# Kernel optimization log

Measured on AMD Instinct MI355X. Metric: run time of the kernel, lower is better.

The kernel has to match this reference:

```python
import jax, jax.numpy as jnp
import numpy as np

N_NODES = 100000


def gcn_conv(x, edge_index, W, b):
    # PyG GCNConv: add self-loops, symmetric normalization, then scatter-add.
    n = x.shape[0]
    loops = jnp.arange(n, dtype=edge_index.dtype)
    src = jnp.concatenate([edge_index[0], loops])
    dst = jnp.concatenate([edge_index[1], loops])
    h = x @ W  # [N, F_out] -- transform before propagate (small GEMM)
    ones = jnp.ones(src.shape[0], dtype=x.dtype)
    deg = jax.ops.segment_sum(ones, dst, num_segments=n)  # in-degree incl. self-loop
    dinv = jnp.where(deg > 0, jax.lax.rsqrt(deg), 0.0)
    norm = dinv[src] * dinv[dst]  # [E+N]
    msg = h[src] * norm[:, None]  # gather + scale, [E+N, F_out]
    out = jax.ops.segment_sum(msg, dst, num_segments=n)  # scatter-add
    return out + b


def setup_inputs() -> dict:
    key = jax.random.key(0)
    k1, k2, k3, k4 = jax.random.split(key, 4)
    d = 128
    x = jax.random.normal(k1, (N_NODES, d), dtype=jnp.float32)
    edge_index = jax.random.randint(k2, (2, 1600000), 0, N_NODES, dtype=jnp.int64)
    scale = 1.0 / np.sqrt(d)
    W1 = jax.random.normal(k3, (d, d), dtype=jnp.float32) * scale
    b1 = jnp.zeros((d,), dtype=jnp.float32)
    W2 = jax.random.normal(k4, (d, d), dtype=jnp.float32) * scale
    b2 = jnp.zeros((d,), dtype=jnp.float32)
    return {"x": x, "edge_index": edge_index, "W1": W1, "b1": b1, "W2": W2, "b2": b2}


def reference(x, edge_index, W1, b1, W2, b2):
    # Layer 1: GCNConv -> relu -> dropout(eval: identity)
    h = jax.nn.relu(gcn_conv(x, edge_index, W1, b1))
    # Layer 2
    h = jax.nn.relu(gcn_conv(h, edge_index, W2, b2))
    return h
```

## Files before the change

### kernel.cpp

```cpp
#include <hip/hip_runtime.h>


#define NFEAT 128
#define BSH 7
#define MAXNB 1024
#define BCAP 4096

typedef __attribute__((ext_vector_type(8))) short s8v;
typedef __attribute__((ext_vector_type(4))) float f4v;

__device__ inline ushort f2bf(float f) {
    union { float f; uint u; } x; x.f = f;
    uint u = x.u;
    return (ushort)((u + 0x7fffu + ((u >> 16) & 1u)) >> 16);
}
__device__ inline float bf16lo(uint u) { union { uint u; float f; } x; x.u = u << 16; return x.f; }
__device__ inline float bf16hi(uint u) { union { uint u; float f; } x; x.u = u & 0xffff0000u; return x.f; }

__device__ inline void upadd(uint4 v, float* a) {
    a[0] += bf16lo(v.x); a[1] += bf16hi(v.x);
    a[2] += bf16lo(v.y); a[3] += bf16hi(v.y);
    a[4] += bf16lo(v.z); a[5] += bf16hi(v.z);
    a[6] += bf16lo(v.w); a[7] += bf16hi(v.w);
}

__global__ __launch_bounds__(256) void k_prep(const float* __restrict__ W1,
                                              const float* __restrict__ W2,
                                              ushort* __restrict__ WT1,
                                              ushort* __restrict__ WT2,
                                              int* __restrict__ gcnt,
                                              ushort* __restrict__ hs, int N) {
    int t = threadIdx.x;
    if (blockIdx.x == 2) {
        for (int i = t; i < MAXNB; i += 256) gcnt[i] = 0;
        if (t < 64) ((uint*)(hs + (size_t)N * NFEAT))[t] = 0;
        return;
    }
    __shared__ float Ls[128][133];
    const float* W = blockIdx.x ? W2 : W1;
    ushort* WT = blockIdx.x ? WT2 : WT1;
#pragma unroll
    for (int i = 0; i < 64; i++) {
        int idx = t + i * 256;
        Ls[idx >> 7][idx & 127] = W[idx];
    }
    __syncthreads();
#pragma unroll
    for (int i = 0; i < 8; i++) {
        int idx = t + i * 256;
        int n = idx >> 4;
        int k8 = (idx & 15) << 3;
        ushort o[8];
#pragma unroll
        for (int j = 0; j < 8; j++) o[j] = f2bf(Ls[k8 + j][n]);
        uint4 pk;
        __builtin_memcpy(&pk, o, 16);
        *(uint4*)&WT[n * 128 + k8] = pk;
    }
}

__global__ __launch_bounds__(256) void k_bscatter(const int* __restrict__ src,
                                                  const int* __restrict__ dst,
                                                  int* __restrict__ gcnt,
                                                  uint* __restrict__ ebuf,
                                                  int E, int NB, int CH) {
    __shared__ int h[MAXNB];
    int t = threadIdx.x;
    for (int i = t; i < NB; i += 256) h[i] = 0;
    __syncthreads();
    int e0 = blockIdx.x * CH;
    int e1 = min(e0 + CH, E);
    for (int e = e0 + t; e < e1; e += 256) atomicAdd(&h[dst[e] >> BSH], 1);
    __syncthreads();
    for (int i = t; i < NB; i += 256) {
        int c = h[i];
        h[i] = c ? (i * BCAP + atomicAdd(&gcnt[i], c)) : 0;
    }
    __syncthreads();
    for (int e = e0 + t; e < e1; e += 256) {
        int d = dst[e];
        int b = d >> BSH;
        int p = atomicAdd(&h[b], 1);
        if (p < (b + 1) * BCAP)
            ebuf[p] = ((uint)src[e] << BSH) | (uint)(d & ((1 << BSH) - 1));
    }
}

__global__ __launch_bounds__(256) void k_fill2(const uint* __restrict__ ebuf,
                                               const int* __restrict__ gcnt,
                                               int* __restrict__ row_ptr,
                                               float* __restrict__ dinv,
                                               int* __restrict__ col,
                                               int N, int E, int NB) {
    __shared__ int cnt[128];
    __shared__ int pre[128];
    __shared__ int sred[256];
    __shared__ int colL[BCAP];
    int b = blockIdx.x;
    int t = threadIdx.x;
    int part = 0;
    for (int j = t; j < b; j += 256) part += gcnt[j];
    sred[t] = part;
    __syncthreads();
    for (int off = 128; off >= 1; off >>= 1) {
        if (t < off) sred[t] += sred[t + off];
        __syncthreads();
    }
    int gb = sred[0];
    int m = min(gcnt[b], BCAP);
    if (t < 128) cnt[t] = 0;
    __syncthreads();
    const uint* eb = ebuf + (size_t)b * BCAP;
    for (int i = t; i < m; i += 256) atomicAdd(&cnt[eb[i] & 127], 1);
    __syncthreads();
    if (t < 128) pre[t] = cnt[t];
    __syncthreads();
    for (int off = 1; off < 128; off <<= 1) {
        int add = (t >= off && t < 128) ? pre[t - off] : 0;
        __syncthreads();
        if (t < 128) pre[t] += add;
        __syncthreads();
    }
    if (t < 128) {
        pre[t] -= cnt[t];
        int node = (b << BSH) + t;
        if (node < N) {
            row_ptr[node] = gb + pre[t];
            dinv[node] = rsqrtf((float)(cnt[t] + 1));
        }
    }
    __syncthreads();
    for (int i = t; i < m; i += 256) {
        uint p = eb[i];
        int pos = atomicAdd(&pre[p & 127], 1);
        colL[pos] = (int)(p >> BSH);
    }
    __syncthreads();
    for (int i = t; i < m; i += 256) col[gb + i] = colL[i];
    if (b == NB - 1 && t == 0) row_ptr[N] = E;
}

__device__ inline ushort* lds_chunk(ushort* base, int r, int c) {
    return base + r * 128 + ((c ^ (r & 15)) << 3);
}

template <bool ABF16>
__global__ __launch_bounds__(256) void k_gemm_mfma(const void* __restrict__ Ap,
                                                   const ushort* __restrict__ WT,
                                                   const float* __restrict__ dinv,
                                                   ushort* __restrict__ hs, int M) {
    __shared__ ushort As[128 * 128];
    __shared__ ushort Bs[128 * 128];
    int t = threadIdx.x;
    int m0 = blockIdx.x * 128;

    {
        const uint4* wt4 = (const uint4*)WT;
#pragma unroll
        for (int i = 0; i < 8; i++) {
            int idx = t + i * 256;
            int n = idx >> 4;
            int c = idx & 15;
            uint4 v = wt4[idx];
            *(uint4*)lds_chunk(Bs, n, c) = v;
        }
    }
    if (ABF16) {
        const ushort* A = (const ushort*)Ap;
#pragma unroll
        for (int i = 0; i < 8; i++) {
            int idx = t + i * 256;
            int r = idx >> 4;
            int c = idx & 15;
            int row = m0 + r;
            uint4 v = make_uint4(0, 0, 0, 0);
            if (row < M) v = *(const uint4*)(A + (size_t)row * NFEAT + (c << 3));
            *(uint4*)lds_chunk(As, r, c) = v;
        }
    } else {
        const float* A = (const float*)Ap;
#pragma unroll
        for (int i = 0; i < 16; i++) {
            int idx = t + i * 256;
            int r = idx >> 5;
            int t5 = idx & 31;
            int c = t5 >> 1;
            int h = t5 & 1;
            int row = m0 + r;
            float4 v = make_float4(0.f, 0.f, 0.f, 0.f);
            if (row < M) v = *(const float4*)(A + (size_t)row * NFEAT + t5 * 4);
            ushort o[4] = {f2bf(v.x), f2bf(v.y), f2bf(v.z), f2bf(v.w)};
            uint2 pk;
            __builtin_memcpy(&pk, o, 8);
            *(uint2*)(lds_chunk(As, r, c) + h * 4) = pk;
        }
    }
    __syncthreads();

    int w = t >> 6, l = t & 63;
    int q = l >> 4, ln = l & 15;
    f4v acc[2][8];
#pragma unroll
    for (int mt = 0; mt < 2; mt++)
#pragma unroll
        for (int nt = 0; nt < 8; nt++) acc[mt][nt] = (f4v){0.f, 0.f, 0.f, 0.f};

#pragma unroll
    for (int ks = 0; ks < 4; ks++) {
        int c = ks * 4 + q;
        s8v a0 = *(s8v*)lds_chunk(As, w * 32 + ln, c);
        s8v a1 = *(s8v*)lds_chunk(As, w * 32 + 16 + ln, c);
#pragma unroll
        for (int nt = 0; nt < 8; nt++) {
            s8v bb = *(s8v*)lds_chunk(Bs, nt * 16 + ln, c);
            acc[0][nt] = __builtin_amdgcn_mfma_f32_16x16x32_bf16(a0, bb, acc[0][nt], 0, 0, 0);
            acc[1][nt] = __builtin_amdgcn_mfma_f32_16x16x32_bf16(a1, bb, acc[1][nt], 0, 0, 0);
        }
    }

#pragma unroll
    for (int mt = 0; mt < 2; mt++) {
#pragma unroll
        for (int r = 0; r < 4; r++) {
            int grow = m0 + w * 32 + mt * 16 + q * 4 + r;
            if (grow < M) {
                float d = dinv[grow];
#pragma unroll
                for (int nt = 0; nt < 8; nt++) {
                    hs[(size_t)grow * NFEAT + nt * 16 + ln] = f2bf(acc[mt][nt][r] * d);
                }
            }
        }
    }
}

template <bool OUT_BF16>
__global__ __launch_bounds__(256) void k_aggregate(const uint4* __restrict__ hs4,
                                                   const int* __restrict__ row_ptr,
                                                   const int* __restrict__ col,
                                                   const float* __restrict__ dinv,
                                                   const float* __restrict__ bias,
                                                   void* __restrict__ outp, int N) {
    int i = blockIdx.x * 4 + (threadIdx.x >> 6);
    if (i >= N) return;
    int lane = threadIdx.x & 63;
    int g = lane >> 4, sub = lane & 15;
    float a[8];
#pragma unroll
    for (int j = 0; j < 8; j++) a[j] = 0.f;
    if (g == 0) upadd(hs4[(size_t)i * 16 + sub], a);
    int s = row_ptr[i], e = row_ptr[i + 1];
    int k = s;
    for (; k + 16 <= e; k += 16) {
        int c0 = col[k + g];
        int c1 = col[k + 4 + g];
        int c2 = col[k + 8 + g];
        int c3 = col[k + 12 + g];
        uint4 v0 = hs4[(size_t)c0 * 16 + sub];
        uint4 v1 = hs4[(size_t)c1 * 16 + sub];
        uint4 v2 = hs4[(size_t)c2 * 16 + sub];
        uint4 v3 = hs4[(size_t)c3 * 16 + sub];
        upadd(v0, a); upadd(v1, a); upadd(v2, a); upadd(v3, a);
    }
    for (; k < e; k += 4) {
        int idx = k + g;
        int c = N;
        if (idx < e) c = col[idx];
        upadd(hs4[(size_t)c * 16 + sub], a);
    }
#pragma unroll
    for (int j = 0; j < 8; j++) {
        a[j] += __shfl_xor(a[j], 16, 64);
        a[j] += __shfl_xor(a[j], 32, 64);
    }
    if (lane < 16) {
        float di = dinv[i];
        const float4* b4 = (const float4*)bias;
        float4 b0 = b4[sub * 2], b1 = b4[sub * 2 + 1];
        float r[8];
        r[0] = fmaxf(fmaf(di, a[0], b0.x), 0.f);
        r[1] = fmaxf(fmaf(di, a[1], b0.y), 0.f);
        r[2] = fmaxf(fmaf(di, a[2], b0.z), 0.f);
        r[3] = fmaxf(fmaf(di, a[3], b0.w), 0.f);
        r[4] = fmaxf(fmaf(di, a[4], b1.x), 0.f);
        r[5] = fmaxf(fmaf(di, a[5], b1.y), 0.f);
        r[6] = fmaxf(fmaf(di, a[6], b1.z), 0.f);
        r[7] = fmaxf(fmaf(di, a[7], b1.w), 0.f);
        if (OUT_BF16) {
            ushort o[8];
#pragma unroll
            for (int j = 0; j < 8; j++) o[j] = f2bf(r[j]);
            uint4 pk;
            __builtin_memcpy(&pk, o, 16);
            ((uint4*)outp)[(size_t)i * 16 + sub] = pk;
        } else {
            float* orow = (float*)outp + (size_t)i * NFEAT + sub * 8;
            *(float4*)orow = make_float4(r[0], r[1], r[2], r[3]);
            *(float4*)(orow + 4) = make_float4(r[4], r[5], r[6], r[7]);
        }
    }
}

extern "C" void kernel_launch(void* const* d_in, const int* in_sizes, int n_in,
                              void* d_out, int out_size, void* d_ws, size_t ws_size,
                              hipStream_t stream) {
    const float* x = (const float*)d_in[0];
    const int* ei = (const int*)d_in[1];
    const float* W1 = (const float*)d_in[2];
    const float* b1 = (const float*)d_in[3];
    const float* W2 = (const float*)d_in[4];
    const float* b2 = (const float*)d_in[5];
    float* out = (float*)d_out;

    const int N = in_sizes[0] / NFEAT;
    const int E = in_sizes[1] / 2;
    const int* src = ei;
    const int* dst = ei + E;
    const int NB = (N + (1 << BSH) - 1) >> BSH;

    char* w = (char*)d_ws;
    size_t off = 0;
    auto alloc = [&](size_t bytes) -> void* {
        void* p = w + off;
        off = (off + bytes + 511) & ~(size_t)511;
        return p;
    };
    ushort* hs = (ushort*)alloc((size_t)(N + 1) * NFEAT * 2);
    ushort* y1 = (ushort*)alloc((size_t)N * NFEAT * 2);
    ushort* WT1 = (ushort*)alloc(128 * 128 * 2);
    ushort* WT2 = (ushort*)alloc(128 * 128 * 2);
    int* row_ptr = (int*)alloc((size_t)(N + 1) * 4);
    float* dinv = (float*)alloc((size_t)N * 4);
    int* col = (int*)alloc((size_t)E * 4);
    uint* ebuf = (uint*)alloc((size_t)NB * BCAP * 4);
    int* gcnt = (int*)alloc((size_t)MAXNB * 4);
    (void)ws_size; (void)n_in; (void)out_size;

    const int CH = 8192;
    const int chBlk = (E + CH - 1) / CH;

    k_prep<<<3, 256, 0, stream>>>(W1, W2, WT1, WT2, gcnt, hs, N);
    k_bscatter<<<chBlk, 256, 0, stream>>>(src, dst, gcnt, ebuf, E, NB, CH);
    k_fill2<<<NB, 256, 0, stream>>>(ebuf, gcnt, row_ptr, dinv, col, N, E, NB);

    const int gemmBlk = (N + 127) / 128;
    const int aggBlk = (N + 3) / 4;

    k_gemm_mfma<false><<<gemmBlk, 256, 0, stream>>>(x, WT1, dinv, hs, N);
    k_aggregate<true><<<aggBlk, 256, 0, stream>>>((const uint4*)hs, row_ptr, col, dinv, b1, y1, N);
    k_gemm_mfma<true><<<gemmBlk, 256, 0, stream>>>(y1, WT2, dinv, hs, N);
    k_aggregate<false><<<aggBlk, 256, 0, stream>>>((const uint4*)hs, row_ptr, col, dinv, b2, out, N);
}
```

Baseline: 323.1 us.

## Load GEMM fragments directly into registers and stage output through LDS

The GEMM no longer stages A and W tiles in shared memory. Each wave loads its A fragments straight from global memory into registers and reads W fragments from global (L2-cached) memory inside the MFMA loop. Results go through a per-wave padded LDS buffer so each row is written back with coalesced 16-byte stores instead of scattered 2-byte stores. This removes the block-wide barrier and LDS load traffic, but relies on the cache for the repeated W reads and uses a waitcnt instead of a barrier for the intra-wave LDS round trip.

```diff
diff --git a/kernel.cpp b/kernel.cpp
--- a/kernel.cpp
+++ b/kernel.cpp
@@ -140,97 +140,80 @@
     if (b == NB - 1 && t == 0) row_ptr[N] = E;
 }
 
-__device__ inline ushort* lds_chunk(ushort* base, int r, int c) {
-    return base + r * 128 + ((c ^ (r & 15)) << 3);
-}
+#define OPITCH 160
 
 template <bool ABF16>
-__global__ __launch_bounds__(256) void k_gemm_mfma(const void* __restrict__ Ap,
-                                                   const ushort* __restrict__ WT,
-                                                   const float* __restrict__ dinv,
-                                                   ushort* __restrict__ hs, int M) {
-    __shared__ ushort As[128 * 128];
-    __shared__ ushort Bs[128 * 128];
+__global__ __launch_bounds__(256) void k_gemm2(const void* __restrict__ Ap,
+                                               const ushort* __restrict__ WT,
+                                               const float* __restrict__ dinv,
+                                               ushort* __restrict__ hs, int M) {
+    __shared__ ushort OutS[4 * 32 * OPITCH];
     int t = threadIdx.x;
-    int m0 = blockIdx.x * 128;
-
-    {
-        const uint4* wt4 = (const uint4*)WT;
-#pragma unroll
-        for (int i = 0; i < 8; i++) {
-            int idx = t + i * 256;
-            int n = idx >> 4;
-            int c = idx & 15;
-            uint4 v = wt4[idx];
-            *(uint4*)lds_chunk(Bs, n, c) = v;
-        }
-    }
-    if (ABF16) {
-        const ushort* A = (const ushort*)Ap;
-#pragma unroll
-        for (int i = 0; i < 8; i++) {
-            int idx = t + i * 256;
-            int r = idx >> 4;
-            int c = idx & 15;
-            int row = m0 + r;
-            uint4 v = make_uint4(0, 0, 0, 0);
-            if (row < M) v = *(const uint4*)(A + (size_t)row * NFEAT + (c << 3));
-            *(uint4*)lds_chunk(As, r, c) = v;
-        }
-    } else {
-        const float* A = (const float*)Ap;
-#pragma unroll
-        for (int i = 0; i < 16; i++) {
-            int idx = t + i * 256;
-            int r = idx >> 5;
-            int t5 = idx & 31;
-            int c = t5 >> 1;
-            int h = t5 & 1;
-            int row = m0 + r;
-            float4 v = make_float4(0.f, 0.f, 0.f, 0.f);
-            if (row < M) v = *(const float4*)(A + (size_t)row * NFEAT + t5 * 4);
-            ushort o[4] = {f2bf(v.x), f2bf(v.y), f2bf(v.z), f2bf(v.w)};
-            uint2 pk;
-            __builtin_memcpy(&pk, o, 8);
-            *(uint2*)(lds_chunk(As, r, c) + h * 4) = pk;
-        }
-    }
-    __syncthreads();
-
     int w = t >> 6, l = t & 63;
     int q = l >> 4, ln = l & 15;
+    int row0 = (blockIdx.x * 4 + w) * 32;
+    if (row0 >= M) return;
+
+    s8v afr[2][4];
+#pragma unroll
+    for (int mt = 0; mt < 2; mt++) {
+        int row = row0 + mt * 16 + ln;
+        if (row >= M) row = M - 1;
+        if (ABF16) {
+            const ushort* A = (const ushort*)Ap + (size_t)row * NFEAT + q * 8;
+#pragma unroll
+            for (int ks = 0; ks < 4; ks++)
+                afr[mt][ks] = *(const s8v*)(A + ks * 32);
+        } else {
+            const float* A = (const float*)Ap + (size_t)row * NFEAT + q * 8;
+#pragma unroll
+            for (int ks = 0; ks < 4; ks++) {
+                float4 f0 = *(const float4*)(A + ks * 32);
+                float4 f1 = *(const float4*)(A + ks * 32 + 4);
+                ushort o[8] = {f2bf(f0.x), f2bf(f0.y), f2bf(f0.z), f2bf(f0.w),
+                               f2bf(f1.x), f2bf(f1.y), f2bf(f1.z), f2bf(f1.w)};
+                __builtin_memcpy(&afr[mt][ks], o, 16);
+            }
+        }
+    }
+
     f4v acc[2][8];
 #pragma unroll
     for (int mt = 0; mt < 2; mt++)
 #pragma unroll
         for (int nt = 0; nt < 8; nt++) acc[mt][nt] = (f4v){0.f, 0.f, 0.f, 0.f};
-
-#pragma unroll
-    for (int ks = 0; ks < 4; ks++) {
-        int c = ks * 4 + q;
-        s8v a0 = *(s8v*)lds_chunk(As, w * 32 + ln, c);
-        s8v a1 = *(s8v*)lds_chunk(As, w * 32 + 16 + ln, c);
-#pragma unroll
-        for (int nt = 0; nt < 8; nt++) {
-            s8v bb = *(s8v*)lds_chunk(Bs, nt * 16 + ln, c);
-            acc[0][nt] = __builtin_amdgcn_mfma_f32_16x16x32_bf16(a0, bb, acc[0][nt], 0, 0, 0);
-            acc[1][nt] = __builtin_amdgcn_mfma_f32_16x16x32_bf16(a1, bb, acc[1][nt], 0, 0, 0);
-        }
-    }
-
+#pragma unroll
+    for (int nt = 0; nt < 8; nt++) {
+        const ushort* Bp = WT + (nt * 16 + ln) * NFEAT + q * 8;
+#pragma unroll
+        for (int ks = 0; ks < 4; ks++) {
+            s8v bfr = *(const s8v*)(Bp + ks * 32);
+            acc[0][nt] = __builtin_amdgcn_mfma_f32_16x16x32_bf16(afr[0][ks], bfr, acc[0][nt], 0, 0, 0);
+            acc[1][nt] = __builtin_amdgcn_mfma_f32_16x16x32_bf16(afr[1][ks], bfr, acc[1][nt], 0, 0, 0);
+        }
+    }
+
+    ushort* ow = OutS + w * 32 * OPITCH;
 #pragma unroll
     for (int mt = 0; mt < 2; mt++) {
 #pragma unroll
         for (int r = 0; r < 4; r++) {
-            int grow = m0 + w * 32 + mt * 16 + q * 4 + r;
-            if (grow < M) {
-                float d = dinv[grow];
-#pragma unroll
-                for (int nt = 0; nt < 8; nt++) {
-                    hs[(size_t)grow * NFEAT + nt * 16 + ln] = f2bf(acc[mt][nt][r] * d);
-                }
-            }
-        }
+            int lrow = mt * 16 + q * 4 + r;
+            int grow = row0 + lrow;
+            float d = (grow < M) ? dinv[grow] : 0.f;
+#pragma unroll
+            for (int nt = 0; nt < 8; nt++)
+                ow[lrow * OPITCH + nt * 16 + ln] = f2bf(acc[mt][nt][r] * d);
+        }
+    }
+    __builtin_amdgcn_s_waitcnt(0);
+#pragma unroll
+    for (int i = 0; i < 8; i++) {
+        int idx = l + i * 64;
+        int r = idx >> 4, c = idx & 15;
+        uint4 v = *(uint4*)(ow + r * OPITCH + c * 8);
+        int grow = row0 + r;
+        if (grow < M) *(uint4*)(hs + (size_t)grow * NFEAT + c * 8) = v;
     }
 }
 
@@ -346,8 +329,8 @@
     const int gemmBlk = (N + 127) / 128;
     const int aggBlk = (N + 3) / 4;
 
-    k_gemm_mfma<false><<<gemmBlk, 256, 0, stream>>>(x, WT1, dinv, hs, N);
+    k_gemm2<false><<<gemmBlk, 256, 0, stream>>>(x, WT1, dinv, hs, N);
     k_aggregate<true><<<aggBlk, 256, 0, stream>>>((const uint4*)hs, row_ptr, col, dinv, b1, y1, N);
-    k_gemm_mfma<true><<<gemmBlk, 256, 0, stream>>>(y1, WT2, dinv, hs, N);
+    k_gemm2<true><<<gemmBlk, 256, 0, stream>>>(y1, WT2, dinv, hs, N);
     k_aggregate<false><<<aggBlk, 256, 0, stream>>>((const uint4*)hs, row_ptr, col, dinv, b2, out, N);
 }
```

Result: slower. 335.9 us (+4.0%).
